# Performance work log

Measured on AMD Instinct MI355X. Metric: run time of the kernel, lower is better.

## Reference

```python
import jax, jax.numpy as jnp
import numpy as np

BLANK = 59  # CFG['pad_phrase'] == blank_index == label pad value
NEG = jnp.float32(-1e30)  # -inf surrogate safe for logaddexp


def setup_inputs() -> dict:
    key = jax.random.key(0)
    k1, k2 = jax.random.split(key)
    B, T, V, L = 1024, 384, 60, 45
    labels = jax.random.randint(k1, (B, L), 0, BLANK, dtype=jnp.int32)
    logits = jax.random.normal(k2, (B, T, V), dtype=jnp.float32)
    return {"labels": labels, "logits": logits}


def _ctc_loss(logits, labels):
    # logits: [B, T, V] (not time-major), labels: [B, L] padded with BLANK
    B, T, V = logits.shape
    L = labels.shape[1]
    S = 2 * L + 1  # extended label length: blanks interleaved

    logp = jax.nn.log_softmax(logits, axis=-1)  # tf.nn.ctc_loss softmaxes internally

    # extended label sequence: [blank, l1, blank, l2, ..., blank]
    ext = jnp.full((B, S), BLANK, dtype=jnp.int32).at[:, 1::2].set(labels)
    # per-step emission log-probs for each extended-label position: [B, T, S]
    emit = jnp.take_along_axis(logp, ext[:, None, :], axis=2)

    # skip transition s-2 -> s allowed iff s >= 2, ext[s] != blank, ext[s] != ext[s-2]
    ext_m2 = jnp.pad(ext[:, :-2], ((0, 0), (2, 0)), constant_values=-1)
    skip_ok = (jnp.arange(S) >= 2) & (ext != BLANK) & (ext != ext_m2)

    # alpha init at t=0: only positions 0 (blank) and 1 (first label) reachable
    alpha0 = jnp.full((B, S), NEG).at[:, 0].set(emit[:, 0, 0]).at[:, 1].set(emit[:, 0, 1])

    def step(alpha, emit_t):
        s1 = jnp.pad(alpha[:, :-1], ((0, 0), (1, 0)), constant_values=NEG)
        s2 = jnp.where(skip_ok, jnp.pad(alpha[:, :-2], ((0, 0), (2, 0)), constant_values=NEG), NEG)
        alpha = jnp.logaddexp(jnp.logaddexp(alpha, s1), s2) + emit_t
        return alpha, None

    emit_tbs = jnp.swapaxes(emit, 0, 1)  # [T, B, S]
    alpha_T, _ = jax.lax.scan(step, alpha0, emit_tbs[1:])

    # label_length = number of non-pad tokens (as in the TF layer)
    label_len = jnp.sum((labels != BLANK).astype(jnp.int32), axis=-1)
    end = 2 * label_len  # index of final blank in extended sequence
    a_blank = jnp.take_along_axis(alpha_T, end[:, None], axis=1)[:, 0]
    a_label = jnp.take_along_axis(alpha_T, jnp.maximum(end - 1, 0)[:, None], axis=1)[:, 0]
    a_label = jnp.where(end > 0, a_label, NEG)
    nll = -jnp.logaddexp(a_blank, a_label)  # [B]
    return jnp.mean(nll)


def reference(labels, logits):
    return _ctc_loss(logits, labels)
```

## Files before the change

kernel.cpp:

```cpp
#include <hip/hip_runtime.h>
#include <hip/hip_fp16.h>

#define BLANKC 59

typedef _Float16 half8 __attribute__((ext_vector_type(8)));
typedef _Float16 half4 __attribute__((ext_vector_type(4)));

#define LDS_FENCE() asm volatile("s_waitcnt lgkmcnt(0)" ::: "memory")

__device__ __forceinline__ float wave_shr1(float x, float fill) {
    int r = __builtin_amdgcn_update_dpp(__float_as_int(fill), __float_as_int(x),
                                        0x138 , 0xF, 0xF, false);
    return __int_as_float(r);
}
__device__ __forceinline__ float wave_shl1(float x, float fill) {
    int r = __builtin_amdgcn_update_dpp(__float_as_int(fill), __float_as_int(x),
                                        0x130 , 0xF, 0xF, false);
    return __int_as_float(r);
}

template <int CTRL>
__device__ __forceinline__ float dpp_fmax(float x) {
    int r = __builtin_amdgcn_update_dpp(__float_as_int(x), __float_as_int(x),
                                        CTRL, 0xF, 0xF, false);
    return fmaxf(x, __int_as_float(r));
}
template <int CTRL>
__device__ __forceinline__ float dpp_addf(float x) {
    int r = __builtin_amdgcn_update_dpp(__float_as_int(x), __float_as_int(x),
                                        CTRL, 0xF, 0xF, false);
    return x + __int_as_float(r);
}
__device__ __forceinline__ float wave_max_bcast(float x) {
    x = dpp_fmax<0x111>(x); x = dpp_fmax<0x112>(x);
    x = dpp_fmax<0x114>(x); x = dpp_fmax<0x118>(x);
    x = dpp_fmax<0x142>(x); x = dpp_fmax<0x143>(x);
    return __int_as_float(__builtin_amdgcn_readlane(__float_as_int(x), 63));
}
__device__ __forceinline__ float wave_sum_bcast(float x) {
    x = dpp_addf<0x111>(x); x = dpp_addf<0x112>(x);
    x = dpp_addf<0x114>(x); x = dpp_addf<0x118>(x);
    x = dpp_addf<0x142>(x); x = dpp_addf<0x143>(x);
    return __int_as_float(__builtin_amdgcn_readlane(__float_as_int(x), 63));
}

#define RS   392
#define SCRS 68

__global__ __launch_bounds__(256)
void ctc_fused(const int* __restrict__ labels, const float* __restrict__ logits,
               float* __restrict__ out, int T, int V, int L, float inv_b) {
    const int b    = blockIdx.x;
    const int tid  = threadIdx.x;
    const int lane = tid & 63;
    const int wid  = tid >> 6;

    __shared__ __align__(16) __half S[46 * RS];
    __shared__ __align__(16) __half scr[2][8][SCRS];
    __shared__ float fa0[64], fa1[64];
    __shared__ int labs[64];
    __shared__ int flags[2];
    __shared__ int esF_s, wdone;

    if (tid < 64) labs[tid] = (tid < L) ? labels[(long)b * L + tid] : BLANKC;
    if (tid == 0) { flags[0] = 0; flags[1] = 0; wdone = 0; }
    __syncthreads();

    if (wid >= 2) {
        const int h  = wid - 2;
        const int tq = lane >> 3;
        const int q  = lane & 7;
        const int c0 = q * 8;
        const bool full = (q < 7);
        const float* src = logits + (long)b * T * V;

        int gl[6], gr[6], gv[6]; bool gok[6];
        #pragma unroll
        for (int k = 0; k < 6; ++k) {
            const int i = lane + (k << 6);
            gok[k] = (i < 368);
            gl[k] = i >> 3; gr[k] = i & 7;
            const int ll = gok[k] ? gl[k] : 0;
            gv[k] = (ll < 45) ? labs[ll] : BLANKC;
        }

        float4 A0, A1{0.f,0.f,0.f,0.f}, B0{0.f,0.f,0.f,0.f}, B1;
        {   const int ch0 = h ? 47 : 0;
            const float* p = src + (ch0 * 8 + tq) * 60 + c0;
            A0 = *(const float4*)p;
            if (full) A1 = *(const float4*)(p + 4);
        }
        for (int pass = 0; pass < 24; ++pass) {
            const int ch = h ? (47 - pass) : pass;
            B1 = float4{0.f,0.f,0.f,0.f};
            if (pass < 23) {
                const int ch2 = h ? (46 - pass) : (pass + 1);
                const float* p = src + (ch2 * 8 + tq) * 60 + c0;
                B0 = *(const float4*)p;
                if (full) B1 = *(const float4*)(p + 4);
            }
            const float e0 = __expf(A0.x), e1 = __expf(A0.y),
                        e2 = __expf(A0.z), e3 = __expf(A0.w);
            float e4 = 0.f, e5 = 0.f, e6 = 0.f, e7 = 0.f;
            if (full) { e4 = __expf(A1.x); e5 = __expf(A1.y);
                        e6 = __expf(A1.z); e7 = __expf(A1.w); }
            float s = ((e0 + e1) + (e2 + e3)) + ((e4 + e5) + (e6 + e7));
            s = dpp_addf<0xB1>(s);
            s = dpp_addf<0x4E>(s);
            s += __shfl_xor(s, 4, 64);
            const float inv = __builtin_amdgcn_rcpf(s);
            const half4 p0 = { (_Float16)(e0 * inv), (_Float16)(e1 * inv),
                               (_Float16)(e2 * inv), (_Float16)(e3 * inv) };
            const half4 p1 = { (_Float16)(e4 * inv), (_Float16)(e5 * inv),
                               (_Float16)(e6 * inv), (_Float16)(e7 * inv) };
            *(half4*)&scr[h][tq][c0]     = p0;
            *(half4*)&scr[h][tq][c0 + 4] = p1;
            LDS_FENCE();

            #pragma unroll
            for (int k = 0; k < 6; ++k) {
                if (gok[k]) {
                    const int cp = ch ^ ((gl[k] >> 3) & 7);
                    S[gl[k] * RS + cp * 8 + gr[k]] = scr[h][gr[k]][gv[k]];
                }
            }
            LDS_FENCE();
            if (lane == 0)
                __hip_atomic_fetch_add(&flags[h], 1, __ATOMIC_RELAXED,
                                       __HIP_MEMORY_SCOPE_WORKGROUP);
            A0 = B0; A1 = B1;
        }
        return;
    }

    const int labL = (lane < L) ? labs[lane] : BLANKC;
    const int labP = (lane >= 1 && lane < L) ? labs[lane - 1] : BLANKC;
    const float skipf = ((lane >= 1) && (lane < L) && (labL != BLANKC) && (labL != labP))
                        ? 1.0f : 0.0f;
    const unsigned long long mk = __ballot((lane < L) && (labL != BLANKC));
    const int len = __popcll(mk);

    const int rl = (lane < 45) ? lane : 45;
    const __half* baseL = &S[rl * RS];
    const __half* baseB = &S[45 * RS];
    const int xL = (rl >> 3) & 7;
    const int xB = 5;

    const half8 hz = {};
    auto loadch = [&](int c, half8& hL, half8& hB) {
        hL = *(const half8*)(baseL + (c ^ xL) * 8);
        hB = *(const half8*)(baseB + (c ^ xB) * 8);
        if (lane >= 45) hL = hz;
        if (lane >= 46) hB = hz;
    };

    const int h = wid;
    int seen = 0;
    auto waitp = [&](int need) {
        while (seen < need) {
            __builtin_amdgcn_s_sleep(1);
            seen = __hip_atomic_load(&flags[h], __ATOMIC_RELAXED,
                                     __HIP_MEMORY_SCOPE_WORKGROUP);
        }
        asm volatile("" ::: "memory");
    };

    if (wid == 0) {
        float a0 = 0.f, a1 = 0.f;
        int esum = 80;
        auto step = [&](float eL, float eB) {
            const float p   = wave_shr1(a1, 0.0f);
            const float t1  = a0 + a1;
            const float na0 = (a0 + p) * eB;
            const float na1 = fmaf(skipf, p, t1) * eL;
            a0 = na0; a1 = na1;
        };
        auto renorm = [&]() {
            const float m = wave_max_bcast(fmaxf(a0, a1));
            const int e = (__float_as_int(m) >> 23) & 0xff;
            int sexp = 207 - e;
            if (sexp > 127) sexp = 127;
            const float sc = __int_as_float((sexp + 127) << 23);
            a0 *= sc; a1 *= sc;
            esum += sexp;
        };
        half8 cL, cB, nL, nB;
        waitp(1); loadch(0, cL, cB);
        for (int c = 0; c < 24; ++c) {
            if (c + 1 < 24) { waitp(c + 2); loadch(c + 1, nL, nB); }
            if (c == 0) {
                a0 = (lane == 0) ? (float)cB[0] * 0x1p80f : 0.f;
                a1 = (lane == 0) ? (float)cL[0] * 0x1p80f : 0.f;
                #pragma unroll
                for (int i = 1; i < 8; ++i) step((float)cL[i], (float)cB[i]);
            } else {
                #pragma unroll
                for (int i = 0; i < 8; ++i) step((float)cL[i], (float)cB[i]);
            }
            renorm();
            cL = nL; cB = nB;
        }
        fa0[lane] = a0;
        fa1[lane] = a1;
        if (lane == 0) esF_s = esum;
        LDS_FENCE();
        if (lane == 0)
            __hip_atomic_store(&wdone, 1, __ATOMIC_RELAXED,
                               __HIP_MEMORY_SCOPE_WORKGROUP);
        return;
    }

    float g0 = (lane == len) ? 0x1p80f : 0.f;
    float g1 = (lane == len - 1) ? 0x1p80f : 0.f;
    int esum = 80;
    auto bstep = [&](float eL, float eB) {
        const float h0 = g0 * eB;
        const float h1 = g1 * eL;
        const float qq = wave_shl1(fmaf(skipf, h1, h0), 0.0f);
        g0 = h0 + h1;
        g1 = h1 + qq;
    };
    auto renormB = [&]() {
        const float m = wave_max_bcast(fmaxf(g0, g1));
        const int e = (__float_as_int(m) >> 23) & 0xff;
        int sexp = 207 - e;
        if (sexp > 127) sexp = 127;
        const float sc = __int_as_float((sexp + 127) << 23);
        g0 *= sc; g1 *= sc;
        esum += sexp;
    };
    half8 cL, cB, nL, nB;
    waitp(1); loadch(47, cL, cB);
    for (int k = 0; k < 24; ++k) {
        if (k + 1 < 24) { waitp(k + 2); loadch(46 - k, nL, nB); }
        #pragma unroll
        for (int i = 7; i >= 0; --i) bstep((float)cL[i], (float)cB[i]);
        renormB();
        cL = nL; cB = nB;
    }

    int d = __hip_atomic_load(&wdone, __ATOMIC_RELAXED, __HIP_MEMORY_SCOPE_WORKGROUP);
    while (!d) {
        __builtin_amdgcn_s_sleep(1);
        d = __hip_atomic_load(&wdone, __ATOMIC_RELAXED, __HIP_MEMORY_SCOPE_WORKGROUP);
    }
    asm volatile("" ::: "memory");
    const float t0 = __log2f(fa0[lane]) + __log2f(g0);
    const float t1 = __log2f(fa1[lane]) + __log2f(g1);
    const float m  = wave_max_bcast(fmaxf(t0, t1));
    const float tt = wave_sum_bcast(exp2f(t0 - m) + exp2f(t1 - m));
    if (lane == 0) {
        const float log2P = m + __log2f(tt) - (float)(esum + esF_s);
        const float nll = -0.69314718055994531f * log2P;
        atomicAdd(out, nll * inv_b);
    }
}

extern "C" void kernel_launch(void* const* d_in, const int* in_sizes, int n_in,
                              void* d_out, int out_size, void* d_ws, size_t ws_size,
                              hipStream_t stream) {
    const int* labels   = (const int*)d_in[0];
    const float* logits = (const float*)d_in[1];
    float* out          = (float*)d_out;
    (void)d_ws; (void)ws_size;

    const int L = 45, V = 60;
    const int B = in_sizes[0] / L;
    const int T = in_sizes[1] / (B * V);

    hipMemsetAsync(out, 0, (size_t)out_size * sizeof(float), stream);
    ctc_fused<<<B, 256, 0, stream>>>(labels, logits, out, T, V, L, 1.0f / (float)B);
}
```

Before: 154.8 us.

## Fuse softmax/gather producer waves into forward/backward recursion waves

Removes the two dedicated producer waves and has each recursion wave compute its own softmax and label gather per 8-step chunk into a small private LDS buffer. This drops the flag-based spin-wait handoff and the large 46x392 shared staging array, and halves the block to 128 threads, so more blocks can fit per CU. In exchange, exp, softmax and gather work now sit serially on each recursion wave's critical path, with only register double-buffered global prefetch left to hide latency.

```diff
diff --git a/kernel.cpp b/kernel.cpp
--- a/kernel.cpp
+++ b/kernel.cpp
@@ -44,10 +44,10 @@
     return __int_as_float(__builtin_amdgcn_readlane(__float_as_int(x), 63));
 }
 
-#define RS   392
 #define SCRS 68
-
-__global__ __launch_bounds__(256)
+#define SDS  24
+
+__global__ __launch_bounds__(128)
 void ctc_fused(const int* __restrict__ labels, const float* __restrict__ logits,
                float* __restrict__ out, int T, int V, int L, float inv_b) {
     const int b    = blockIdx.x;
@@ -55,114 +55,68 @@
     const int lane = tid & 63;
     const int wid  = tid >> 6;
 
-    __shared__ __align__(16) __half S[46 * RS];
     __shared__ __align__(16) __half scr[2][8][SCRS];
+    __shared__ __align__(16) __half Sd[2][46 * SDS];
     __shared__ float fa0[64], fa1[64];
-    __shared__ int labs[64];
-    __shared__ int flags[2];
-    __shared__ int esF_s, wdone;
-
-    if (tid < 64) labs[tid] = (tid < L) ? labels[(long)b * L + tid] : BLANKC;
-    if (tid == 0) { flags[0] = 0; flags[1] = 0; wdone = 0; }
+    __shared__ int   labs[2][64];
+    __shared__ int   esF_s, wdone;
+
+    labs[wid][lane] = (lane < L) ? labels[(long)b * L + lane] : BLANKC;
+    if (tid == 0) wdone = 0;
     __syncthreads();
 
-    if (wid >= 2) {
-        const int h  = wid - 2;
-        const int tq = lane >> 3;
-        const int q  = lane & 7;
-        const int c0 = q * 8;
-        const bool full = (q < 7);
-        const float* src = logits + (long)b * T * V;
-
-        int gl[6], gr[6], gv[6]; bool gok[6];
-        #pragma unroll
-        for (int k = 0; k < 6; ++k) {
-            const int i = lane + (k << 6);
-            gok[k] = (i < 368);
-            gl[k] = i >> 3; gr[k] = i & 7;
-            const int ll = gok[k] ? gl[k] : 0;
-            gv[k] = (ll < 45) ? labs[ll] : BLANKC;
-        }
-
-        float4 A0, A1{0.f,0.f,0.f,0.f}, B0{0.f,0.f,0.f,0.f}, B1;
-        {   const int ch0 = h ? 47 : 0;
-            const float* p = src + (ch0 * 8 + tq) * 60 + c0;
-            A0 = *(const float4*)p;
-            if (full) A1 = *(const float4*)(p + 4);
-        }
-        for (int pass = 0; pass < 24; ++pass) {
-            const int ch = h ? (47 - pass) : pass;
-            B1 = float4{0.f,0.f,0.f,0.f};
-            if (pass < 23) {
-                const int ch2 = h ? (46 - pass) : (pass + 1);
-                const float* p = src + (ch2 * 8 + tq) * 60 + c0;
-                B0 = *(const float4*)p;
-                if (full) B1 = *(const float4*)(p + 4);
-            }
-            const float e0 = __expf(A0.x), e1 = __expf(A0.y),
-                        e2 = __expf(A0.z), e3 = __expf(A0.w);
-            float e4 = 0.f, e5 = 0.f, e6 = 0.f, e7 = 0.f;
-            if (full) { e4 = __expf(A1.x); e5 = __expf(A1.y);
-                        e6 = __expf(A1.z); e7 = __expf(A1.w); }
-            float s = ((e0 + e1) + (e2 + e3)) + ((e4 + e5) + (e6 + e7));
-            s = dpp_addf<0xB1>(s);
-            s = dpp_addf<0x4E>(s);
-            s += __shfl_xor(s, 4, 64);
-            const float inv = __builtin_amdgcn_rcpf(s);
-            const half4 p0 = { (_Float16)(e0 * inv), (_Float16)(e1 * inv),
-                               (_Float16)(e2 * inv), (_Float16)(e3 * inv) };
-            const half4 p1 = { (_Float16)(e4 * inv), (_Float16)(e5 * inv),
-                               (_Float16)(e6 * inv), (_Float16)(e7 * inv) };
-            *(half4*)&scr[h][tq][c0]     = p0;
-            *(half4*)&scr[h][tq][c0 + 4] = p1;
-            LDS_FENCE();
-
-            #pragma unroll
-            for (int k = 0; k < 6; ++k) {
-                if (gok[k]) {
-                    const int cp = ch ^ ((gl[k] >> 3) & 7);
-                    S[gl[k] * RS + cp * 8 + gr[k]] = scr[h][gr[k]][gv[k]];
-                }
-            }
-            LDS_FENCE();
-            if (lane == 0)
-                __hip_atomic_fetch_add(&flags[h], 1, __ATOMIC_RELAXED,
-                                       __HIP_MEMORY_SCOPE_WORKGROUP);
-            A0 = B0; A1 = B1;
-        }
-        return;
-    }
-
-    const int labL = (lane < L) ? labs[lane] : BLANKC;
-    const int labP = (lane >= 1 && lane < L) ? labs[lane - 1] : BLANKC;
+    const int* mylab = labs[wid];
+
+    const int tq = lane >> 3;
+    const int q  = lane & 7;
+    const int c0 = q * 8;
+    const bool full = (q < 7);
+    const float* src = logits + (long)b * T * V;
+
+    int gl[6], gr[6], gv[6]; bool gok[6];
+    #pragma unroll
+    for (int k = 0; k < 6; ++k) {
+        const int i = lane + (k << 6);
+        gok[k] = (i < 368);
+        gl[k] = i >> 3; gr[k] = i & 7;
+        gv[k] = (gok[k] && gl[k] < 45) ? mylab[gl[k]] : BLANKC;
+    }
+
+    const int labL = (lane < L) ? mylab[lane] : BLANKC;
+    const int labP = (lane >= 1 && lane < L) ? mylab[lane - 1] : BLANKC;
     const float skipf = ((lane >= 1) && (lane < L) && (labL != BLANKC) && (labL != labP))
                         ? 1.0f : 0.0f;
     const unsigned long long mk = __ballot((lane < L) && (labL != BLANKC));
     const int len = __popcll(mk);
 
     const int rl = (lane < 45) ? lane : 45;
-    const __half* baseL = &S[rl * RS];
-    const __half* baseB = &S[45 * RS];
-    const int xL = (rl >> 3) & 7;
-    const int xB = 5;
-
+    const __half* rowL = &Sd[wid][rl * SDS];
+    const __half* rowB = &Sd[wid][45 * SDS];
     const half8 hz = {};
-    auto loadch = [&](int c, half8& hL, half8& hB) {
-        hL = *(const half8*)(baseL + (c ^ xL) * 8);
-        hB = *(const half8*)(baseB + (c ^ xB) * 8);
-        if (lane >= 45) hL = hz;
-        if (lane >= 46) hB = hz;
-    };
-
-    const int h = wid;
-    int seen = 0;
-    auto waitp = [&](int need) {
-        while (seen < need) {
-            __builtin_amdgcn_s_sleep(1);
-            seen = __hip_atomic_load(&flags[h], __ATOMIC_RELAXED,
-                                     __HIP_MEMORY_SCOPE_WORKGROUP);
-        }
-        asm volatile("" ::: "memory");
+
+    auto ld = [&](int ch, float4& P0, float4& P1) {
+        const float* p = src + (ch * 8 + tq) * 60 + c0;
+        P0 = *(const float4*)p;
+        if (full) P1 = *(const float4*)(p + 4);
+    };
+    auto smx_gather = [&](float e0, float e1, float e2, float e3,
+                          float e4, float e5, float e6, float e7) {
+        float s = ((e0 + e1) + (e2 + e3)) + ((e4 + e5) + (e6 + e7));
+        s = dpp_addf<0xB1>(s);
+        s = dpp_addf<0x4E>(s);
+        s += __shfl_xor(s, 4, 64);
+        const float inv = __builtin_amdgcn_rcpf(s);
+        const half4 p0 = { (_Float16)(e0 * inv), (_Float16)(e1 * inv),
+                           (_Float16)(e2 * inv), (_Float16)(e3 * inv) };
+        const half4 p1 = { (_Float16)(e4 * inv), (_Float16)(e5 * inv),
+                           (_Float16)(e6 * inv), (_Float16)(e7 * inv) };
+        *(half4*)&scr[wid][tq][c0]     = p0;
+        *(half4*)&scr[wid][tq][c0 + 4] = p1;
+        LDS_FENCE();
+        #pragma unroll
+        for (int k = 0; k < 6; ++k)
+            if (gok[k]) Sd[wid][gl[k] * SDS + gr[k]] = scr[wid][gr[k]][gv[k]];
+        LDS_FENCE();
     };
 
     if (wid == 0) {
@@ -184,11 +138,19 @@
             a0 *= sc; a1 *= sc;
             esum += sexp;
         };
-        half8 cL, cB, nL, nB;
-        waitp(1); loadch(0, cL, cB);
-        for (int c = 0; c < 24; ++c) {
-            if (c + 1 < 24) { waitp(c + 2); loadch(c + 1, nL, nB); }
-            if (c == 0) {
+        auto body = [&](int ch, int pre, float4& P0, float4& P1, bool first) {
+            const float e0 = __expf(P0.x), e1 = __expf(P0.y),
+                        e2 = __expf(P0.z), e3 = __expf(P0.w);
+            float e4 = 0.f, e5 = 0.f, e6 = 0.f, e7 = 0.f;
+            if (full) { e4 = __expf(P1.x); e5 = __expf(P1.y);
+                        e6 = __expf(P1.z); e7 = __expf(P1.w); }
+            if (pre >= 0) ld(pre, P0, P1);
+            smx_gather(e0, e1, e2, e3, e4, e5, e6, e7);
+            half8 cL = *(const half8*)rowL;
+            half8 cB = *(const half8*)rowB;
+            if (lane >= 45) cL = hz;
+            if (lane >= 46) cB = hz;
+            if (first) {
                 a0 = (lane == 0) ? (float)cB[0] * 0x1p80f : 0.f;
                 a1 = (lane == 0) ? (float)cL[0] * 0x1p80f : 0.f;
                 #pragma unroll
@@ -198,7 +160,12 @@
                 for (int i = 0; i < 8; ++i) step((float)cL[i], (float)cB[i]);
             }
             renorm();
-            cL = nL; cB = nB;
+        };
+        float4 X0, X1{0.f,0.f,0.f,0.f}, Y0, Y1{0.f,0.f,0.f,0.f};
+        ld(0, X0, X1); ld(1, Y0, Y1);
+        for (int c = 0; c < 24; c += 2) {
+            body(c,     (c + 2 < 24) ? c + 2 : -1, X0, X1, c == 0);
+            body(c + 1, (c + 3 < 24) ? c + 3 : -1, Y0, Y1, false);
         }
         fa0[lane] = a0;
         fa1[lane] = a1;
@@ -229,14 +196,27 @@
         g0 *= sc; g1 *= sc;
         esum += sexp;
     };
-    half8 cL, cB, nL, nB;
-    waitp(1); loadch(47, cL, cB);
-    for (int k = 0; k < 24; ++k) {
-        if (k + 1 < 24) { waitp(k + 2); loadch(46 - k, nL, nB); }
+    auto bodyb = [&](int ch, int pre, float4& P0, float4& P1) {
+        const float e0 = __expf(P0.x), e1 = __expf(P0.y),
+                    e2 = __expf(P0.z), e3 = __expf(P0.w);
+        float e4 = 0.f, e5 = 0.f, e6 = 0.f, e7 = 0.f;
+        if (full) { e4 = __expf(P1.x); e5 = __expf(P1.y);
+                    e6 = __expf(P1.z); e7 = __expf(P1.w); }
+        if (pre >= 0) ld(pre, P0, P1);
+        smx_gather(e0, e1, e2, e3, e4, e5, e6, e7);
+        half8 cL = *(const half8*)rowL;
+        half8 cB = *(const half8*)rowB;
+        if (lane >= 45) cL = hz;
+        if (lane >= 46) cB = hz;
         #pragma unroll
         for (int i = 7; i >= 0; --i) bstep((float)cL[i], (float)cB[i]);
         renormB();
-        cL = nL; cB = nB;
+    };
+    float4 X0, X1{0.f,0.f,0.f,0.f}, Y0, Y1{0.f,0.f,0.f,0.f};
+    ld(47, X0, X1); ld(46, Y0, Y1);
+    for (int k = 0; k < 24; k += 2) {
+        bodyb(47 - k,       (k + 2 < 24) ? 47 - (k + 2) : -1, X0, X1);
+        bodyb(47 - (k + 1), (k + 3 < 24) ? 47 - (k + 3) : -1, Y0, Y1);
     }
 
     int d = __hip_atomic_load(&wdone, __ATOMIC_RELAXED, __HIP_MEMORY_SCOPE_WORKGROUP);
@@ -269,5 +249,5 @@
     const int T = in_sizes[1] / (B * V);
 
     hipMemsetAsync(out, 0, (size_t)out_size * sizeof(float), stream);
-    ctc_fused<<<B, 256, 0, stream>>>(labels, logits, out, T, V, L, 1.0f / (float)B);
-}
+    ctc_fused<<<B, 128, 0, stream>>>(labels, logits, out, T, V, L, 1.0f / (float)B);
+}
```

New measurement: 155.3 us. No clear change (+0.3%).
